# Optimization experiments

Measured on AMD Instinct MI355X. Metric: run time of the kernel, lower is better.

The kernel has to match this reference:

```python
import jax, jax.numpy as jnp
import numpy as np

D_IN = 1024
D_OUT = 1024
NUM_HEADS = 16
HEAD_DIM = D_OUT // NUM_HEADS


def setup_inputs() -> dict:
    key = jax.random.key(0)
    ks = jax.random.split(key, 6)
    s = 1.0 / np.sqrt(D_IN)
    return {
        "x": jax.random.normal(ks[0], (4, 2048, D_IN), dtype=jnp.float32),
        "Wq": jax.random.uniform(ks[1], (D_IN, D_OUT), jnp.float32, -s, s),
        "Wk": jax.random.uniform(ks[2], (D_IN, D_OUT), jnp.float32, -s, s),
        "Wv": jax.random.uniform(ks[3], (D_IN, D_OUT), jnp.float32, -s, s),
        "Wo": jax.random.uniform(ks[4], (D_OUT, D_OUT), jnp.float32, -s, s),
        "bo": jax.random.uniform(ks[5], (D_OUT,), jnp.float32, -s, s),
    }


def reference(x, Wq, Wk, Wv, Wo, bo):
    b, n, _ = x.shape
    # QKV projections -> [b, h, n, d]
    def heads(t):
        return t.reshape(b, n, NUM_HEADS, HEAD_DIM).transpose(0, 2, 1, 3)
    q = heads(x @ Wq)
    k = heads(x @ Wk)
    v = heads(x @ Wv)
    # scaled scores with causal mask
    scores = jnp.einsum("bhqd,bhkd->bhqk", q, k) / jnp.sqrt(jnp.float32(HEAD_DIM))
    causal = jnp.tril(jnp.ones((n, n), dtype=bool))  # True = keep
    scores = jnp.where(causal, scores, -jnp.inf)
    attn = jax.nn.softmax(scores, axis=-1)  # dropout p=0.0 -> identity
    ctx = jnp.einsum("bhqk,bhkd->bhqd", attn, v)
    ctx = ctx.transpose(0, 2, 1, 3).reshape(b, n, D_OUT)
    return ctx @ Wo + bo
```

## Files before the change

kernel.cpp:

```cpp
#include <hip/hip_runtime.h>
#include <hip/hip_bf16.h>
#include <math.h>

typedef __attribute__((ext_vector_type(8))) __bf16 bf16x8;
typedef __attribute__((ext_vector_type(4))) __bf16 bf16x4;
typedef __attribute__((ext_vector_type(4))) float f32x4;
typedef __attribute__((ext_vector_type(4))) short short4_t;

#define D_MODEL 1024
#define SEQ     2048
#define BATCH   4
#define NH      16
#define HD      64
#define MROWS   (BATCH * SEQ)

#define SCALE_LOG2E 0.18033688011112042f

__device__ __forceinline__ void gld_lds16(const __bf16* g, __bf16* l) {
  __builtin_amdgcn_global_load_lds(
      (const __attribute__((address_space(1))) void*)g,
      (__attribute__((address_space(3))) void*)l, 16, 0, 0);
}

__global__ __launch_bounds__(256) void cvt_x(const float* __restrict__ in,
                                             __bf16* __restrict__ out) {
  int i = (blockIdx.x * 256 + threadIdx.x) * 4;
  float4 f = *(const float4*)(in + i);
  bf16x4 o;
  o.x = (__bf16)f.x; o.y = (__bf16)f.y; o.z = (__bf16)f.z; o.w = (__bf16)f.w;
  *(bf16x4*)(out + i) = o;
}

__global__ __launch_bounds__(256) void cvt_wt(const float* __restrict__ W,
                                              __bf16* __restrict__ Wt) {
  __shared__ __bf16 t[32][33];
  int tx = threadIdx.x, ty = threadIdx.y;
  int n0 = blockIdx.x * 32, k0 = blockIdx.y * 32;
#pragma unroll
  for (int j = 0; j < 32; j += 8)
    t[ty + j][tx] = (__bf16)W[(size_t)(k0 + ty + j) * D_MODEL + n0 + tx];
  __syncthreads();
#pragma unroll
  for (int j = 0; j < 32; j += 8)
    Wt[(size_t)(n0 + ty + j) * D_MODEL + k0 + tx] = t[tx][ty + j];
}

template <int EPI>
__global__ __launch_bounds__(256) void gemm_bt(const __bf16* __restrict__ A,
                                               const __bf16* __restrict__ Bt,
                                               const float* __restrict__ bias,
                                               void* __restrict__ Cout) {
  constexpr int Kd = 1024;
  constexpr bool SWAP = (EPI != 1);
  __shared__ __bf16 As[128 * 32];
  __shared__ __bf16 Bs[128 * 32];
  const int tid = threadIdx.x;
  const int lane = tid & 63;
  const int w = tid >> 6;
  const int quad = lane >> 4, l16 = lane & 15;
  const int wr = w >> 1, wc = w & 1;
  const int tm = blockIdx.y * 128, tn = blockIdx.x * 128;

  f32x4 acc[4][4] = {};

  const int u0 = (w * 2) * 64 + lane;
  const int u1 = u0 + 64;
  const int rA0 = u0 >> 2, kofs0 = (u0 & 3) * 8;
  const int rA1 = u1 >> 2, kofs1 = (u1 & 3) * 8;
  const __bf16* gA0 = A + (size_t)(tm + rA0) * Kd + kofs0;
  const __bf16* gA1 = A + (size_t)(tm + rA1) * Kd + kofs1;
  const __bf16* gB0 = Bt + (size_t)(tn + rA0) * Kd + kofs0;
  const __bf16* gB1 = Bt + (size_t)(tn + rA1) * Kd + kofs1;
  __bf16* lA0 = As + (w * 2 + 0) * 512;
  __bf16* lA1 = As + (w * 2 + 1) * 512;
  __bf16* lB0 = Bs + (w * 2 + 0) * 512;
  __bf16* lB1 = Bs + (w * 2 + 1) * 512;

  for (int k0 = 0; k0 < Kd; k0 += 32) {
    gld_lds16(gA0 + k0, lA0);
    gld_lds16(gA1 + k0, lA1);
    gld_lds16(gB0 + k0, lB0);
    gld_lds16(gB1 + k0, lB1);
    __syncthreads();
    bf16x8 af[4], bfr[4];
#pragma unroll
    for (int t = 0; t < 4; ++t) {
      af[t]  = *(const bf16x8*)&As[(wr * 64 + t * 16 + l16) * 32 + quad * 8];
      bfr[t] = *(const bf16x8*)&Bs[(wc * 64 + t * 16 + l16) * 32 + quad * 8];
    }
#pragma unroll
    for (int mt = 0; mt < 4; ++mt)
#pragma unroll
      for (int nt = 0; nt < 4; ++nt) {
        if constexpr (SWAP)
          acc[mt][nt] = __builtin_amdgcn_mfma_f32_16x16x32_bf16(
              bfr[nt], af[mt], acc[mt][nt], 0, 0, 0);
        else
          acc[mt][nt] = __builtin_amdgcn_mfma_f32_16x16x32_bf16(
              af[mt], bfr[nt], acc[mt][nt], 0, 0, 0);
      }
    __syncthreads();
  }

#pragma unroll
  for (int mt = 0; mt < 4; ++mt)
#pragma unroll
    for (int nt = 0; nt < 4; ++nt) {
      if constexpr (EPI == 2) {
        int gm  = tm + wr * 64 + mt * 16 + l16;
        int gn0 = tn + wc * 64 + nt * 16 + quad * 4;
        float4 bv = *(const float4*)&bias[gn0];
        float4 o;
        o.x = acc[mt][nt][0] + bv.x;
        o.y = acc[mt][nt][1] + bv.y;
        o.z = acc[mt][nt][2] + bv.z;
        o.w = acc[mt][nt][3] + bv.w;
        *(float4*)&((float*)Cout)[(size_t)gm * 1024 + gn0] = o;
      } else if constexpr (EPI == 0) {
        int gm = tm + wr * 64 + mt * 16 + l16;
        int f0 = tn + wc * 64 + nt * 16 + quad * 4;
        int which = f0 >> 10, col = f0 & 1023;
        int b = gm >> 11, nn = gm & 2047, h = col >> 6, d = col & 63;
        float s = (which == 0) ? SCALE_LOG2E : 1.0f;
        bf16x4 o;
        o[0] = (__bf16)(acc[mt][nt][0] * s);
        o[1] = (__bf16)(acc[mt][nt][1] * s);
        o[2] = (__bf16)(acc[mt][nt][2] * s);
        o[3] = (__bf16)(acc[mt][nt][3] * s);
        __bf16* op = (__bf16*)Cout + (size_t)which * (BATCH * SEQ * (size_t)D_MODEL) +
                     ((size_t)(b * NH + h) * SEQ + nn) * HD + d;
        *(bf16x4*)op = o;
      } else {
        int gm0 = tm + wr * 64 + mt * 16 + quad * 4;
        int gn  = tn + wc * 64 + nt * 16 + l16;
        int b = gm0 >> 11, nn0 = gm0 & 2047, h = gn >> 6, d = gn & 63;
        bf16x4 o;
        o[0] = (__bf16)acc[mt][nt][0];
        o[1] = (__bf16)acc[mt][nt][1];
        o[2] = (__bf16)acc[mt][nt][2];
        o[3] = (__bf16)acc[mt][nt][3];
        __bf16* op = (__bf16*)Cout + ((size_t)(b * NH + h) * HD + d) * SEQ + nn0;
        *(bf16x4*)op = o;
      }
    }
}

__global__ __launch_bounds__(256, 2) void attn(const __bf16* __restrict__ Q,
                                               const __bf16* __restrict__ K,
                                               const __bf16* __restrict__ Vt,
                                               __bf16* __restrict__ ctx) {
  const int tid = threadIdx.x;
  const int lane = tid & 63, w = tid >> 6;
  const int quad = lane >> 4, l16 = lane & 15;
  const int pr = blockIdx.x;
  const int bh = blockIdx.y;
  const int tile0 = pr, tile1 = 15 - pr;
  const __bf16* qb = Q + (size_t)bh * SEQ * HD;
  const __bf16* kb = K + (size_t)bh * SEQ * HD;
  const __bf16* vb = Vt + (size_t)bh * HD * SEQ;

  __shared__ __bf16 KsAll[2 * 4096];
  __shared__ __bf16 VsAll[2 * 4096];

  const int qmin[2] = {tile0 * 128 + w * 32, tile1 * 128 + w * 32};

  bf16x8 aq[2][2][2];
#pragma unroll
  for (int p = 0; p < 2; ++p)
#pragma unroll
    for (int qq = 0; qq < 2; ++qq)
#pragma unroll
      for (int kk = 0; kk < 2; ++kk)
        aq[p][qq][kk] = *(const bf16x8*)(qb + (size_t)(qmin[p] + qq * 16 + l16) * HD +
                                         kk * 32 + quad * 8);

  f32x4 acc[2][2][4] = {};
  float lsum[2][2] = {};

  const int u0 = w * 128 + lane;
  const int u1 = u0 + 64;
  const int kOffG0 = ((u0 >> 2) & 63) * HD + (u0 >> 8) * 32 + (u0 & 3) * 8;
  const int kOffG1 = ((u1 >> 2) & 63) * HD + (u1 >> 8) * 32 + (u1 & 3) * 8;
  const int vd0 = u0 >> 3, vd1 = u1 >> 3;
  const int vOffG0 = vd0 * SEQ + (((u0 & 7) ^ (vd0 & 7)) * 8);
  const int vOffG1 = vd1 * SEQ + (((u1 & 7) ^ (vd1 & 7)) * 8);

  auto stage = [&](int k0s, int bufsel) {
    __bf16* Kb = KsAll + bufsel * 4096;
    __bf16* Vb = VsAll + bufsel * 4096;
    gld_lds16(kb + (size_t)k0s * HD + kOffG0, Kb + u0 * 8);
    gld_lds16(kb + (size_t)k0s * HD + kOffG1, Kb + u1 * 8);
    gld_lds16(vb + k0s + vOffG0, Vb + u0 * 8);
    gld_lds16(vb + k0s + vOffG1, Vb + u1 * 8);
  };

  const int nIter = 2 * tile1 + 2;
  stage(0, 0);

  for (int it = 0; it < nIter; ++it) {
    __syncthreads();
    if (it + 1 < nIter) stage((it + 1) * 64, (it + 1) & 1);

    const int k0 = it * 64;
    if (k0 <= qmin[1] + 31) {
      const __bf16* Kb = KsAll + (it & 1) * 4096;
      const __bf16* Vb = VsAll + (it & 1) * 4096;

      bf16x8 bk[4][2];
#pragma unroll
      for (int kt = 0; kt < 4; ++kt)
#pragma unroll
        for (int kk = 0; kk < 2; ++kk)
          bk[kt][kk] = *(const bf16x8*)&Kb[kk * 2048 + (kt * 16 + l16) * 32 + quad * 8];

      short4_t vf[4][4];
#pragma unroll
      for (int kt = 0; kt < 4; ++kt)
#pragma unroll
        for (int cd = 0; cd < 4; ++cd)
          vf[kt][cd] = *(const short4_t*)&Vb[(cd * 16 + l16) * 64 +
                                             (((kt * 2 + (quad >> 1)) ^ (l16 & 7)) * 8) +
                                             (quad & 1) * 4];

#pragma unroll
      for (int p = 0; p < 2; ++p) {
        if (k0 > qmin[p] + 31) continue;
        f32x4 St[4][2] = {};
#pragma unroll
        for (int kt = 0; kt < 4; ++kt)
#pragma unroll
          for (int qq = 0; qq < 2; ++qq) {
            St[kt][qq] = __builtin_amdgcn_mfma_f32_16x16x32_bf16(
                bk[kt][0], aq[p][qq][0], St[kt][qq], 0, 0, 0);
            St[kt][qq] = __builtin_amdgcn_mfma_f32_16x16x32_bf16(
                bk[kt][1], aq[p][qq][1], St[kt][qq], 0, 0, 0);
          }
        const bool full = (k0 + 63 <= qmin[p]);
#pragma unroll
        for (int kt = 0; kt < 4; ++kt)
#pragma unroll
          for (int qq = 0; qq < 2; ++qq) {
            float e0 = __builtin_amdgcn_exp2f(St[kt][qq][0]);
            float e1 = __builtin_amdgcn_exp2f(St[kt][qq][1]);
            float e2 = __builtin_amdgcn_exp2f(St[kt][qq][2]);
            float e3 = __builtin_amdgcn_exp2f(St[kt][qq][3]);
            if (!full) {
              int kg = k0 + kt * 16 + quad * 4;
              int qg = qmin[p] + qq * 16 + l16;
              if (kg + 0 > qg) e0 = 0.f;
              if (kg + 1 > qg) e1 = 0.f;
              if (kg + 2 > qg) e2 = 0.f;
              if (kg + 3 > qg) e3 = 0.f;
            }
            lsum[p][qq] += (e0 + e1) + (e2 + e3);
            short4_t ap;
            ap[0] = __builtin_bit_cast(short, (__bf16)e0);
            ap[1] = __builtin_bit_cast(short, (__bf16)e1);
            ap[2] = __builtin_bit_cast(short, (__bf16)e2);
            ap[3] = __builtin_bit_cast(short, (__bf16)e3);
#pragma unroll
            for (int cd = 0; cd < 4; ++cd)
              acc[p][qq][cd] = __builtin_amdgcn_mfma_f32_16x16x16bf16_1k(
                  ap, vf[kt][cd], acc[p][qq][cd], 0, 0, 0);
          }
      }
    }
  }

  const int bb = bh >> 4, hh = bh & 15;
#pragma unroll
  for (int p = 0; p < 2; ++p) {
#pragma unroll
    for (int qq = 0; qq < 2; ++qq) {
      float s = lsum[p][qq];
      s += __shfl_xor(s, 16);
      s += __shfl_xor(s, 32);
      float rinv[4];
#pragma unroll
      for (int i = 0; i < 4; ++i)
        rinv[i] = 1.0f / __shfl(s, (lane & 48) + quad * 4 + i);
#pragma unroll
      for (int c = 0; c < 4; ++c)
#pragma unroll
        for (int i = 0; i < 4; ++i) {
          int q = qmin[p] + qq * 16 + quad * 4 + i;
          float o = acc[p][qq][c][i] * rinv[i];
          ctx[((size_t)(bb * SEQ + q)) * D_MODEL + hh * HD + c * 16 + l16] = (__bf16)o;
        }
    }
  }
}

extern "C" void kernel_launch(void* const* d_in, const int* in_sizes, int n_in,
                              void* d_out, int out_size, void* d_ws, size_t ws_size,
                              hipStream_t stream) {
  const float* x  = (const float*)d_in[0];
  const float* Wq = (const float*)d_in[1];
  const float* Wk = (const float*)d_in[2];
  const float* Wv = (const float*)d_in[3];
  const float* Wo = (const float*)d_in[4];
  const float* bo = (const float*)d_in[5];
  float* out = (float*)d_out;
  char* ws = (char*)d_ws;
  const size_t MB = 1024 * 1024;
  __bf16* xb   = (__bf16*)(ws);
  __bf16* Wqkv = (__bf16*)(ws + 16 * MB);
  __bf16* Wot  = (__bf16*)(ws + 22 * MB);
  __bf16* Qh   = (__bf16*)(ws + 24 * MB);
  __bf16* Kh   = (__bf16*)(ws + 40 * MB);
  __bf16* Vth  = (__bf16*)(ws + 56 * MB);
  __bf16* ctx  = xb;

  cvt_x<<<MROWS * D_MODEL / (256 * 4), 256, 0, stream>>>(x, xb);
  dim3 tb(32, 8);
  cvt_wt<<<dim3(32, 32), tb, 0, stream>>>(Wq, Wqkv);
  cvt_wt<<<dim3(32, 32), tb, 0, stream>>>(Wk, Wqkv + 1024 * 1024);
  cvt_wt<<<dim3(32, 32), tb, 0, stream>>>(Wv, Wqkv + 2 * 1024 * 1024);
  cvt_wt<<<dim3(32, 32), tb, 0, stream>>>(Wo, Wot);

  gemm_bt<0><<<dim3(16, 64), 256, 0, stream>>>(xb, Wqkv, nullptr, Qh);
  gemm_bt<1><<<dim3(8, 64), 256, 0, stream>>>(xb, Wqkv + 2 * 1024 * 1024, nullptr, Vth);

  attn<<<dim3(8, BATCH * NH), 256, 0, stream>>>(Qh, Kh, Vth, ctx);

  gemm_bt<2><<<dim3(8, 64), 256, 0, stream>>>(ctx, Wot, bo, out);
}
```

Baseline: 272.4 us.

## Double-buffer GEMM LDS tiles and XOR-swizzle K tile in attention

The projection GEMM now keeps two LDS buffers for the A and B tiles. It issues the global-to-LDS load for the next K step before computing on the current one, so memory latency overlaps with MFMA work and one barrier per iteration is removed. The attention kernel's K tile staging and reads now use an XOR swizzle on the 8-element column groups to cut LDS bank conflicts. The cost is doubled GEMM LDS use, which may lower occupancy.

```diff
diff --git a/kernel.cpp b/kernel.cpp
--- a/kernel.cpp
+++ b/kernel.cpp
@@ -52,8 +52,8 @@
                                                void* __restrict__ Cout) {
   constexpr int Kd = 1024;
   constexpr bool SWAP = (EPI != 1);
-  __shared__ __bf16 As[128 * 32];
-  __shared__ __bf16 Bs[128 * 32];
+  __shared__ __bf16 As[2][128 * 32];
+  __shared__ __bf16 Bs[2][128 * 32];
   const int tid = threadIdx.x;
   const int lane = tid & 63;
   const int w = tid >> 6;
@@ -71,22 +71,29 @@
   const __bf16* gA1 = A + (size_t)(tm + rA1) * Kd + kofs1;
   const __bf16* gB0 = Bt + (size_t)(tn + rA0) * Kd + kofs0;
   const __bf16* gB1 = Bt + (size_t)(tn + rA1) * Kd + kofs1;
-  __bf16* lA0 = As + (w * 2 + 0) * 512;
-  __bf16* lA1 = As + (w * 2 + 1) * 512;
-  __bf16* lB0 = Bs + (w * 2 + 0) * 512;
-  __bf16* lB1 = Bs + (w * 2 + 1) * 512;
-
+  const int ldst0 = (w * 2 + 0) * 512;
+  const int ldst1 = (w * 2 + 1) * 512;
+
+  auto stageg = [&](int k0s, int buf) {
+    gld_lds16(gA0 + k0s, &As[buf][ldst0]);
+    gld_lds16(gA1 + k0s, &As[buf][ldst1]);
+    gld_lds16(gB0 + k0s, &Bs[buf][ldst0]);
+    gld_lds16(gB1 + k0s, &Bs[buf][ldst1]);
+  };
+
+  stageg(0, 0);
+  __syncthreads();
+
+  int cur = 0;
+#pragma unroll 2
   for (int k0 = 0; k0 < Kd; k0 += 32) {
-    gld_lds16(gA0 + k0, lA0);
-    gld_lds16(gA1 + k0, lA1);
-    gld_lds16(gB0 + k0, lB0);
-    gld_lds16(gB1 + k0, lB1);
-    __syncthreads();
+    if (k0 + 32 < Kd) stageg(k0 + 32, cur ^ 1);
+
     bf16x8 af[4], bfr[4];
 #pragma unroll
     for (int t = 0; t < 4; ++t) {
-      af[t]  = *(const bf16x8*)&As[(wr * 64 + t * 16 + l16) * 32 + quad * 8];
-      bfr[t] = *(const bf16x8*)&Bs[(wc * 64 + t * 16 + l16) * 32 + quad * 8];
+      af[t]  = *(const bf16x8*)&As[cur][(wr * 64 + t * 16 + l16) * 32 + quad * 8];
+      bfr[t] = *(const bf16x8*)&Bs[cur][(wc * 64 + t * 16 + l16) * 32 + quad * 8];
     }
 #pragma unroll
     for (int mt = 0; mt < 4; ++mt)
@@ -100,6 +107,7 @@
               af[mt], bfr[nt], acc[mt][nt], 0, 0, 0);
       }
     __syncthreads();
+    cur ^= 1;
   }
 
 #pragma unroll
@@ -179,11 +187,14 @@
 
   const int u0 = w * 128 + lane;
   const int u1 = u0 + 64;
-  const int kOffG0 = ((u0 >> 2) & 63) * HD + (u0 >> 8) * 32 + (u0 & 3) * 8;
-  const int kOffG1 = ((u1 >> 2) & 63) * HD + (u1 >> 8) * 32 + (u1 & 3) * 8;
+  const int kOffG0 = ((u0 >> 2) & 63) * HD + (u0 >> 8) * 32 +
+                     (((u0 & 3) ^ ((u0 >> 3) & 3)) * 8);
+  const int kOffG1 = ((u1 >> 2) & 63) * HD + (u1 >> 8) * 32 +
+                     (((u1 & 3) ^ ((u1 >> 3) & 3)) * 8);
   const int vd0 = u0 >> 3, vd1 = u1 >> 3;
   const int vOffG0 = vd0 * SEQ + (((u0 & 7) ^ (vd0 & 7)) * 8);
   const int vOffG1 = vd1 * SEQ + (((u1 & 7) ^ (vd1 & 7)) * 8);
+  const int ksw = (quad ^ ((l16 >> 1) & 3)) * 8;
 
   auto stage = [&](int k0s, int bufsel) {
     __bf16* Kb = KsAll + bufsel * 4096;
@@ -211,7 +222,7 @@
       for (int kt = 0; kt < 4; ++kt)
 #pragma unroll
         for (int kk = 0; kk < 2; ++kk)
-          bk[kt][kk] = *(const bf16x8*)&Kb[kk * 2048 + (kt * 16 + l16) * 32 + quad * 8];
+          bk[kt][kk] = *(const bf16x8*)&Kb[kk * 2048 + (kt * 16 + l16) * 32 + ksw];
 
       short4_t vf[4][4];
 #pragma unroll
```

Result: slower. 284.2 us (+4.3%).

## Triple-buffer GEMM LDS tiles with async global-to-LDS prefetch

Applied to the files above, without the earlier changes.

The bf16 GEMM mainloop changes from a single LDS buffer with two barriers per k-step to a 3-stage ring buffer. Direct global-to-LDS loads are issued two tiles ahead, and each step uses one vmcnt wait plus one barrier. This is meant to hide global load latency behind MFMA work and halve barrier count. It triples the LDS footprint (48KB per block), which may reduce occupancy, and relies on hand-written waitcnt ordering being correct.

```diff
diff --git a/kernel.cpp b/kernel.cpp
--- a/kernel.cpp
+++ b/kernel.cpp
@@ -51,9 +51,10 @@
                                                const float* __restrict__ bias,
                                                void* __restrict__ Cout) {
   constexpr int Kd = 1024;
+  constexpr int NT = Kd / 32;
   constexpr bool SWAP = (EPI != 1);
-  __shared__ __bf16 As[128 * 32];
-  __shared__ __bf16 Bs[128 * 32];
+  __shared__ __bf16 As[3 * 4096];
+  __shared__ __bf16 Bs[3 * 4096];
   const int tid = threadIdx.x;
   const int lane = tid & 63;
   const int w = tid >> 6;
@@ -71,22 +72,24 @@
   const __bf16* gA1 = A + (size_t)(tm + rA1) * Kd + kofs1;
   const __bf16* gB0 = Bt + (size_t)(tn + rA0) * Kd + kofs0;
   const __bf16* gB1 = Bt + (size_t)(tn + rA1) * Kd + kofs1;
-  __bf16* lA0 = As + (w * 2 + 0) * 512;
-  __bf16* lA1 = As + (w * 2 + 1) * 512;
-  __bf16* lB0 = Bs + (w * 2 + 0) * 512;
-  __bf16* lB1 = Bs + (w * 2 + 1) * 512;
-
-  for (int k0 = 0; k0 < Kd; k0 += 32) {
-    gld_lds16(gA0 + k0, lA0);
-    gld_lds16(gA1 + k0, lA1);
-    gld_lds16(gB0 + k0, lB0);
-    gld_lds16(gB1 + k0, lB1);
-    __syncthreads();
+  const int ldst0 = (w * 2 + 0) * 512;
+  const int ldst1 = (w * 2 + 1) * 512;
+
+  auto stageg = [&](int k0s, int bi) {
+    gld_lds16(gA0 + k0s, As + bi * 4096 + ldst0);
+    gld_lds16(gA1 + k0s, As + bi * 4096 + ldst1);
+    gld_lds16(gB0 + k0s, Bs + bi * 4096 + ldst0);
+    gld_lds16(gB1 + k0s, Bs + bi * 4096 + ldst1);
+  };
+
+  auto compute = [&](int bi) {
+    const __bf16* Ab = As + bi * 4096;
+    const __bf16* Bb = Bs + bi * 4096;
     bf16x8 af[4], bfr[4];
 #pragma unroll
     for (int t = 0; t < 4; ++t) {
-      af[t]  = *(const bf16x8*)&As[(wr * 64 + t * 16 + l16) * 32 + quad * 8];
-      bfr[t] = *(const bf16x8*)&Bs[(wc * 64 + t * 16 + l16) * 32 + quad * 8];
+      af[t]  = *(const bf16x8*)&Ab[(wr * 64 + t * 16 + l16) * 32 + quad * 8];
+      bfr[t] = *(const bf16x8*)&Bb[(wc * 64 + t * 16 + l16) * 32 + quad * 8];
     }
 #pragma unroll
     for (int mt = 0; mt < 4; ++mt)
@@ -99,8 +102,31 @@
           acc[mt][nt] = __builtin_amdgcn_mfma_f32_16x16x32_bf16(
               af[mt], bfr[nt], acc[mt][nt], 0, 0, 0);
       }
-    __syncthreads();
+  };
+
+  stageg(0, 0);
+  stageg(32, 1);
+
+  int bi = 0, bs = 2;
+#pragma unroll 3
+  for (int i = 0; i < NT - 2; ++i) {
+    asm volatile("s_waitcnt vmcnt(4)" ::: "memory");
+    __builtin_amdgcn_s_barrier();
+    __builtin_amdgcn_sched_barrier(0);
+    stageg((i + 2) * 32, bs);
+    compute(bi);
+    bi = (bi == 2) ? 0 : bi + 1;
+    bs = (bs == 2) ? 0 : bs + 1;
   }
+  asm volatile("s_waitcnt vmcnt(4)" ::: "memory");
+  __builtin_amdgcn_s_barrier();
+  __builtin_amdgcn_sched_barrier(0);
+  compute(bi);
+  bi = (bi == 2) ? 0 : bi + 1;
+  asm volatile("s_waitcnt vmcnt(0)" ::: "memory");
+  __builtin_amdgcn_s_barrier();
+  __builtin_amdgcn_sched_barrier(0);
+  compute(bi);
 
 #pragma unroll
   for (int mt = 0; mt < 4; ++mt)
```

After: 283.6 us. 4.1% more time.

## Double-buffer GEMM with 256x128 tiles, 512 threads, and merge weight conversions

Applied to the files above, without the earlier changes.

The projection GEMM now uses 512-thread blocks covering 256x128 output tiles with a K-step of 64. Global-to-LDS loads are double-buffered so the next tile loads while MFMAs run on the current one, and there is one barrier per iteration instead of two. The four weight transpose/convert launches are merged into one 3D-grid launch to cut launch overhead. In exchange, LDS use rises to about 96KB per block and the grid has half as many blocks, which may lower occupancy and hurt load balance.

```diff
diff --git a/kernel.cpp b/kernel.cpp
--- a/kernel.cpp
+++ b/kernel.cpp
@@ -31,10 +31,17 @@
   *(bf16x4*)(out + i) = o;
 }
 
-__global__ __launch_bounds__(256) void cvt_wt(const float* __restrict__ W,
-                                              __bf16* __restrict__ Wt) {
+__global__ __launch_bounds__(256) void cvt_wt4(const float* __restrict__ W0,
+                                               const float* __restrict__ W1,
+                                               const float* __restrict__ W2,
+                                               const float* __restrict__ W3,
+                                               __bf16* __restrict__ Wqkv,
+                                               __bf16* __restrict__ Wot) {
   __shared__ __bf16 t[32][33];
   int tx = threadIdx.x, ty = threadIdx.y;
+  int z = blockIdx.z;
+  const float* W = (z == 0) ? W0 : (z == 1) ? W1 : (z == 2) ? W2 : W3;
+  __bf16* Wt = (z < 3) ? (Wqkv + (size_t)z * 1024 * 1024) : Wot;
   int n0 = blockIdx.x * 32, k0 = blockIdx.y * 32;
 #pragma unroll
   for (int j = 0; j < 32; j += 8)
@@ -46,60 +53,79 @@
 }
 
 template <int EPI>
-__global__ __launch_bounds__(256) void gemm_bt(const __bf16* __restrict__ A,
-                                               const __bf16* __restrict__ Bt,
-                                               const float* __restrict__ bias,
-                                               void* __restrict__ Cout) {
+__global__ __launch_bounds__(512, 2) void gemm_bt(const __bf16* __restrict__ A,
+                                                  const __bf16* __restrict__ Bt,
+                                                  const float* __restrict__ bias,
+                                                  void* __restrict__ Cout) {
   constexpr int Kd = 1024;
+  constexpr int NT = Kd / 64;
   constexpr bool SWAP = (EPI != 1);
-  __shared__ __bf16 As[128 * 32];
-  __shared__ __bf16 Bs[128 * 32];
+  __shared__ __bf16 As[2][256 * 64];
+  __shared__ __bf16 Bs[2][128 * 64];
   const int tid = threadIdx.x;
   const int lane = tid & 63;
   const int w = tid >> 6;
   const int quad = lane >> 4, l16 = lane & 15;
   const int wr = w >> 1, wc = w & 1;
-  const int tm = blockIdx.y * 128, tn = blockIdx.x * 128;
+  const int tm = blockIdx.y * 256, tn = blockIdx.x * 128;
 
   f32x4 acc[4][4] = {};
 
-  const int u0 = (w * 2) * 64 + lane;
-  const int u1 = u0 + 64;
-  const int rA0 = u0 >> 2, kofs0 = (u0 & 3) * 8;
-  const int rA1 = u1 >> 2, kofs1 = (u1 & 3) * 8;
-  const __bf16* gA0 = A + (size_t)(tm + rA0) * Kd + kofs0;
-  const __bf16* gA1 = A + (size_t)(tm + rA1) * Kd + kofs1;
-  const __bf16* gB0 = Bt + (size_t)(tn + rA0) * Kd + kofs0;
-  const __bf16* gB1 = Bt + (size_t)(tn + rA1) * Kd + kofs1;
-  __bf16* lA0 = As + (w * 2 + 0) * 512;
-  __bf16* lA1 = As + (w * 2 + 1) * 512;
-  __bf16* lB0 = Bs + (w * 2 + 0) * 512;
-  __bf16* lB1 = Bs + (w * 2 + 1) * 512;
-
-  for (int k0 = 0; k0 < Kd; k0 += 32) {
-    gld_lds16(gA0 + k0, lA0);
-    gld_lds16(gA1 + k0, lA1);
-    gld_lds16(gB0 + k0, lB0);
-    gld_lds16(gB1 + k0, lB1);
+  const __bf16* pA[4]; int dA[4];
+#pragma unroll
+  for (int j = 0; j < 4; ++j) {
+    int u = j * 512 + tid;
+    int r = (u >> 2) & 255;
+    int ko = (u >> 10) * 32 + (u & 3) * 8;
+    pA[j] = A + (size_t)(tm + r) * Kd + ko;
+    dA[j] = u * 8;
+  }
+  const __bf16* pB[2]; int dB[2];
+#pragma unroll
+  for (int j = 0; j < 2; ++j) {
+    int u = j * 512 + tid;
+    int r = (u >> 2) & 127;
+    int ko = (u >> 9) * 32 + (u & 3) * 8;
+    pB[j] = Bt + (size_t)(tn + r) * Kd + ko;
+    dB[j] = u * 8;
+  }
+
+  auto stageg = [&](int k0s, int bf) {
+#pragma unroll
+    for (int j = 0; j < 4; ++j) gld_lds16(pA[j] + k0s, &As[bf][dA[j]]);
+#pragma unroll
+    for (int j = 0; j < 2; ++j) gld_lds16(pB[j] + k0s, &Bs[bf][dB[j]]);
+  };
+
+  stageg(0, 0);
+  __syncthreads();
+
+  int buf = 0;
+#pragma unroll 2
+  for (int t = 0; t < NT; ++t) {
+    if (t + 1 < NT) stageg((t + 1) * 64, buf ^ 1);
+#pragma unroll
+    for (int kk = 0; kk < 2; ++kk) {
+      bf16x8 af[4], bfr[4];
+#pragma unroll
+      for (int x = 0; x < 4; ++x) {
+        af[x]  = *(const bf16x8*)&As[buf][kk * 8192 + (wr * 64 + x * 16 + l16) * 32 + quad * 8];
+        bfr[x] = *(const bf16x8*)&Bs[buf][kk * 4096 + (wc * 64 + x * 16 + l16) * 32 + quad * 8];
+      }
+#pragma unroll
+      for (int mt = 0; mt < 4; ++mt)
+#pragma unroll
+        for (int nt = 0; nt < 4; ++nt) {
+          if constexpr (SWAP)
+            acc[mt][nt] = __builtin_amdgcn_mfma_f32_16x16x32_bf16(
+                bfr[nt], af[mt], acc[mt][nt], 0, 0, 0);
+          else
+            acc[mt][nt] = __builtin_amdgcn_mfma_f32_16x16x32_bf16(
+                af[mt], bfr[nt], acc[mt][nt], 0, 0, 0);
+        }
+    }
     __syncthreads();
-    bf16x8 af[4], bfr[4];
-#pragma unroll
-    for (int t = 0; t < 4; ++t) {
-      af[t]  = *(const bf16x8*)&As[(wr * 64 + t * 16 + l16) * 32 + quad * 8];
-      bfr[t] = *(const bf16x8*)&Bs[(wc * 64 + t * 16 + l16) * 32 + quad * 8];
-    }
-#pragma unroll
-    for (int mt = 0; mt < 4; ++mt)
-#pragma unroll
-      for (int nt = 0; nt < 4; ++nt) {
-        if constexpr (SWAP)
-          acc[mt][nt] = __builtin_amdgcn_mfma_f32_16x16x32_bf16(
-              bfr[nt], af[mt], acc[mt][nt], 0, 0, 0);
-        else
-          acc[mt][nt] = __builtin_amdgcn_mfma_f32_16x16x32_bf16(
-              af[mt], bfr[nt], acc[mt][nt], 0, 0, 0);
-      }
-    __syncthreads();
+    buf ^= 1;
   }
 
 #pragma unroll
@@ -312,16 +338,12 @@
   __bf16* ctx  = xb;
 
   cvt_x<<<MROWS * D_MODEL / (256 * 4), 256, 0, stream>>>(x, xb);
-  dim3 tb(32, 8);
-  cvt_wt<<<dim3(32, 32), tb, 0, stream>>>(Wq, Wqkv);
-  cvt_wt<<<dim3(32, 32), tb, 0, stream>>>(Wk, Wqkv + 1024 * 1024);
-  cvt_wt<<<dim3(32, 32), tb, 0, stream>>>(Wv, Wqkv + 2 * 1024 * 1024);
-  cvt_wt<<<dim3(32, 32), tb, 0, stream>>>(Wo, Wot);
-
-  gemm_bt<0><<<dim3(16, 64), 256, 0, stream>>>(xb, Wqkv, nullptr, Qh);
-  gemm_bt<1><<<dim3(8, 64), 256, 0, stream>>>(xb, Wqkv + 2 * 1024 * 1024, nullptr, Vth);
+  cvt_wt4<<<dim3(32, 32, 4), dim3(32, 8), 0, stream>>>(Wq, Wk, Wv, Wo, Wqkv, Wot);
+
+  gemm_bt<0><<<dim3(16, 32), 512, 0, stream>>>(xb, Wqkv, nullptr, Qh);
+  gemm_bt<1><<<dim3(8, 32), 512, 0, stream>>>(xb, Wqkv + 2 * 1024 * 1024, nullptr, Vth);
 
   attn<<<dim3(8, BATCH * NH), 256, 0, stream>>>(Qh, Kh, Vth, ctx);
 
-  gemm_bt<2><<<dim3(8, 64), 256, 0, stream>>>(ctx, Wot, bo, out);
-}
+  gemm_bt<2><<<dim3(8, 32), 512, 0, stream>>>(ctx, Wot, bo, out);
+}
```

Measured after the change: 282.5 us. 1.04x slower.
